# Optimization experiments

Measured on AMD Instinct MI355X. Metric: run time of the kernel, lower is better.

Reference implementation:

```python
import jax, jax.numpy as jnp
import numpy as np

B, T, D = 4, 2048, 512
H, DK = 4, 16
MU = 1.0


def _xavier(key, shape):
    lim = float(np.sqrt(6.0 / (shape[0] + shape[1])))
    return jax.random.uniform(key, shape, jnp.float32, -lim, lim)


def setup_inputs() -> dict:
    key = jax.random.key(0)
    ks = jax.random.split(key, 9)
    x = jax.random.normal(ks[0], (B, T, D), jnp.float32)
    Wq = _xavier(ks[1], (D, H * DK))
    Wk = _xavier(ks[2], (D, H * DK))
    Wv = _xavier(ks[3], (D, H * DK))
    # W_a is zero-initialized in the module; use small random values so the
    # decay path is exercised non-trivially.
    Wa = 0.02 * jax.random.normal(ks[4], (D, H), jnp.float32)
    ba = 0.02 * jax.random.normal(ks[5], (H,), jnp.float32)
    Wg = 0.02 * jax.random.normal(ks[6], (D, H * DK), jnp.float32)
    bg = jnp.zeros((H * DK,), jnp.float32)
    Wo = _xavier(ks[7], (H * DK, D))
    return {"x": x, "Wq": Wq, "Wk": Wk, "Wv": Wv, "Wa": Wa, "ba": ba,
            "Wg": Wg, "bg": bg, "Wo": Wo}


def reference(x, Wq, Wk, Wv, Wa, ba, Wg, bg, Wo):
    b_, t_, _ = x.shape
    q = (x @ Wq).reshape(b_, t_, H, DK)
    k = (x @ Wk).reshape(b_, t_, H, DK)
    v = (x @ Wv).reshape(b_, t_, H, DK)
    # bid b_s = <q_s, k_s>/sqrt(dk); decay a_s = -softplus(x W_a + c_a) <= 0
    bid = jnp.sum(q * k, axis=-1) / np.sqrt(DK)      # (B, T, H)
    a = -jax.nn.softplus(x @ Wa + ba)                # (B, T, H)
    # Closed form of the sequential scan:
    #   scores[t, s] = bid[s] + sum_{r=s+1..t} a[r] = (bid[s] - cumA[s]) + cumA[t]
    # Row-constant cumA[t] cancels in the softmax, so the attention weights are
    # a causal softmax over mu * (bid[s] - cumA[s]).
    cumA = jnp.cumsum(a, axis=1)                     # (B, T, H)
    lg = (bid - cumA).transpose(0, 2, 1)             # (B, H, S_keys)
    mask = jnp.tril(jnp.ones((t_, t_), bool))        # keys s <= query t
    scores = jnp.where(mask[None, None], MU * lg[:, :, None, :], -jnp.inf)
    w = jax.nn.softmax(scores, axis=-1)              # (B, H, T, S)
    y = jnp.einsum('bhts,bshd->bthd', w, v)          # (B, T, H, DK)
    gate = jax.nn.sigmoid(x @ Wg + bg).reshape(b_, t_, H, DK)
    y = (y * gate).reshape(b_, t_, H * DK)
    return y @ Wo
```

## Files before the change

### kernel.cpp

```cpp
#include <hip/hip_runtime.h>
#include <math.h>

#define B_    4
#define T_    2048
#define D_    512
#define H_    4
#define ROWS_ 8192
#define CHSZ_ 128
#define NCHK_ 16

typedef unsigned short ushort_t;
typedef unsigned int   uint_t;
typedef __attribute__((ext_vector_type(8))) __bf16         bfx8;
typedef __attribute__((ext_vector_type(8))) unsigned short u16x8;
typedef __attribute__((ext_vector_type(4))) float          fx4;

__device__ __forceinline__ ushort_t f2bf(float f) {
    union { float f; uint_t u; } v; v.f = f;
    return (ushort_t)((v.u + 0x7FFFu + ((v.u >> 16) & 1u)) >> 16);
}
__device__ __forceinline__ float bf2f(ushort_t u) {
    union { uint_t u; float f; } v; v.u = ((uint_t)u) << 16; return v.f;
}

__global__ __launch_bounds__(256) void prep_pack(const float* __restrict__ x,
                                                 const float* __restrict__ Wa,
                                                 const float* __restrict__ ba,
                                                 const float* __restrict__ Wq,
                                                 const float* __restrict__ Wk,
                                                 const float* __restrict__ Wv,
                                                 const float* __restrict__ Wg,
                                                 const float* __restrict__ Wo,
                                                 ushort_t* __restrict__ xbf,
                                                 float* __restrict__ Aarr,
                                                 ushort_t* __restrict__ WcatT2,
                                                 ushort_t* __restrict__ WoT) {
    const int blk = blockIdx.x;
    if (blk < 2048) {
        const int wave = threadIdx.x >> 6, lane = threadIdx.x & 63;
        const int row = blk * 4 + wave;
        const float* xp = x + (size_t)row * D_ + lane * 8;
        float4 f0 = *(const float4*)xp;
        float4 f1 = *(const float4*)(xp + 4);
        float xv[8] = {f0.x, f0.y, f0.z, f0.w, f1.x, f1.y, f1.z, f1.w};

        u16x8 u;
        #pragma unroll
        for (int j = 0; j < 8; j++) u[j] = f2bf(xv[j]);
        *(u16x8*)(xbf + (size_t)row * D_ + lane * 8) = u;

        float a0 = 0.f, a1 = 0.f, a2 = 0.f, a3 = 0.f;
        #pragma unroll
        for (int j = 0; j < 8; j++) {
            float4 w = *(const float4*)&Wa[(size_t)(lane * 8 + j) * 4];
            a0 = fmaf(xv[j], w.x, a0);
            a1 = fmaf(xv[j], w.y, a1);
            a2 = fmaf(xv[j], w.z, a2);
            a3 = fmaf(xv[j], w.w, a3);
        }
        #pragma unroll
        for (int off = 32; off; off >>= 1) {
            a0 += __shfl_xor(a0, off);
            a1 += __shfl_xor(a1, off);
            a2 += __shfl_xor(a2, off);
            a3 += __shfl_xor(a3, off);
        }
        if (lane == 0) {
            float z[4] = {a0 + ba[0], a1 + ba[1], a2 + ba[2], a3 + ba[3]};
            float r[4];
            #pragma unroll
            for (int h = 0; h < 4; h++)
                r[h] = -(fmaxf(z[h], 0.f) + log1pf(expf(-fabsf(z[h]))));
            *(float4*)&Aarr[(size_t)row * 4] = make_float4(r[0], r[1], r[2], r[3]);
        }
    } else {
        int idx = (blk - 2048) * 256 + threadIdx.x;
        if (idx < 256 * 512) {
            int n = idx >> 9, d = idx & 511;
            int h = n >> 6, r = n & 63, part = r >> 4, j = r & 15;
            int col = h * 16 + j;
            const float* W = (part == 0) ? Wq : (part == 1) ? Wk : (part == 2) ? Wv : Wg;
            WcatT2[idx] = f2bf(W[(size_t)d * 64 + col]);
        } else {
            int r = idx - 256 * 512;
            int n = r >> 6, k = r & 63;
            WoT[r] = f2bf(Wo[(size_t)k * 512 + n]);
        }
    }
}

__global__ __launch_bounds__(256) void gemm_scanA(const ushort_t* __restrict__ xbf,
                                                  const ushort_t* __restrict__ WcatT2,
                                                  const float* __restrict__ Aarr,
                                                  float* __restrict__ stateWS,
                                                  float* __restrict__ chunkSum,
                                                  ushort_t* __restrict__ gBuf) {
    __shared__ ushort_t As[128 * 72];
    __shared__ ushort_t Bs[64 * 72];
    __shared__ float s_a0;
    __shared__ float s_wmax[2];
    __shared__ float s_tot[17];

    const int rc = blockIdx.x & 63;
    const int h  = blockIdx.x >> 6;
    const int m0 = rc * 128;
    const int n0 = h * 64;
    const int b  = rc >> 4, chunk = rc & 15;
    const int bh = b * 4 + h;

    const int tid = threadIdx.x;
    const int wave = tid >> 6, lane = tid & 63;
    const int fr = lane & 15, quad = lane >> 4;
    const int sr = tid >> 3, sc = (tid & 7) * 8;

    fx4 acc[2][4];
    #pragma unroll
    for (int i = 0; i < 2; i++)
        #pragma unroll
        for (int j = 0; j < 4; j++) acc[i][j] = (fx4)0.f;

    u16x8 ra[4], rb[2];
    #pragma unroll
    for (int s = 0; s < 4; s++)
        ra[s] = *(const u16x8*)(xbf + (size_t)(m0 + s * 32 + sr) * D_ + sc);
    #pragma unroll
    for (int s = 0; s < 2; s++)
        rb[s] = *(const u16x8*)(WcatT2 + (size_t)(n0 + s * 32 + sr) * D_ + sc);

    for (int it = 0; it < 8; it++) {
        #pragma unroll
        for (int s = 0; s < 4; s++) *(u16x8*)&As[(s * 32 + sr) * 72 + sc] = ra[s];
        #pragma unroll
        for (int s = 0; s < 2; s++) *(u16x8*)&Bs[(s * 32 + sr) * 72 + sc] = rb[s];
        __syncthreads();
        if (it < 7) {
            const int k0 = (it + 1) * 64;
            #pragma unroll
            for (int s = 0; s < 4; s++)
                ra[s] = *(const u16x8*)(xbf + (size_t)(m0 + s * 32 + sr) * D_ + k0 + sc);
            #pragma unroll
            for (int s = 0; s < 2; s++)
                rb[s] = *(const u16x8*)(WcatT2 + (size_t)(n0 + s * 32 + sr) * D_ + k0 + sc);
        }
        #pragma unroll
        for (int ks = 0; ks < 64; ks += 32) {
            bfx8 af[2], bfr[4];
            #pragma unroll
            for (int mi = 0; mi < 2; mi++)
                af[mi] = *(const bfx8*)&As[(wave * 32 + mi * 16 + fr) * 72 + ks + quad * 8];
            #pragma unroll
            for (int ni = 0; ni < 4; ni++)
                bfr[ni] = *(const bfx8*)&Bs[(ni * 16 + fr) * 72 + ks + quad * 8];
            #pragma unroll
            for (int mi = 0; mi < 2; mi++)
                #pragma unroll
                for (int ni = 0; ni < 4; ni++)
                    acc[mi][ni] = __builtin_amdgcn_mfma_f32_16x16x32_bf16(af[mi], bfr[ni], acc[mi][ni], 0, 0, 0);
        }
        __syncthreads();
    }

    #pragma unroll
    for (int mi = 0; mi < 2; mi++)
        #pragma unroll
        for (int ni = 0; ni < 4; ni++)
            #pragma unroll
            for (int r = 0; r < 4; r++) {
                int rl = wave * 32 + mi * 16 + quad * 4 + r;
                int cl = ni * 16 + fr;
                As[rl * 72 + cl] = f2bf(acc[mi][ni][r]);
            }
    __syncthreads();

    const bool active = (tid < 128);
    float bid = 0.f, a = 0.f;
    float v[16];
    if (active) {
        const ushort_t* ct = &As[tid * 72];
        u16x8 q0 = *(const u16x8*)(ct +  0), q1 = *(const u16x8*)(ct +  8);
        u16x8 k0 = *(const u16x8*)(ct + 16), k1 = *(const u16x8*)(ct + 24);
        u16x8 v0 = *(const u16x8*)(ct + 32), v1 = *(const u16x8*)(ct + 40);
        #pragma unroll
        for (int j = 0; j < 8; j++) {
            bid = fmaf(bf2f(q0[j]), bf2f(k0[j]), bid);
            bid = fmaf(bf2f(q1[j]), bf2f(k1[j]), bid);
            v[j]     = bf2f(v0[j]);
            v[8 + j] = bf2f(v1[j]);
        }
        bid *= 0.25f;
        a = Aarr[(size_t)(m0 + tid) * 4 + h];
    }

    float ca = a;
    #pragma unroll
    for (int off = 1; off < 64; off <<= 1) {
        float up = __shfl_up(ca, off);
        if (lane >= off) ca += up;
    }
    if (tid == 63) s_a0 = ca;
    __syncthreads();
    if (active && wave == 1) ca += s_a0;

    float lg = bid - ca;

    float Mw = active ? lg : -1e30f;
    #pragma unroll
    for (int off = 32; off; off >>= 1) Mw = fmaxf(Mw, __shfl_xor(Mw, off));
    if (active && lane == 0) s_wmax[wave] = Mw;
    __syncthreads();
    const float M0 = s_wmax[0], M1 = s_wmax[1];
    const float Mc = fmaxf(M0, M1);

    float d = active ? __expf(lg - Mw) : 0.f;
    float n[16];
    #pragma unroll
    for (int j = 0; j < 16; j++) n[j] = d * v[j];
    #pragma unroll
    for (int off = 1; off < 64; off <<= 1) {
        float ud = __shfl_up(d, off);
        float un[16];
        #pragma unroll
        for (int j = 0; j < 16; j++) un[j] = __shfl_up(n[j], off);
        if (lane >= off) {
            d += ud;
            #pragma unroll
            for (int j = 0; j < 16; j++) n[j] += un[j];
        }
    }
    if (tid == 63) {
        s_tot[0] = d;
        #pragma unroll
        for (int j = 0; j < 16; j++) s_tot[1 + j] = n[j];
    }
    __syncthreads();
    if (active && wave == 1) {
        float al = __expf(M0 - Mc), be = __expf(M1 - Mc);
        d = s_tot[0] * al + d * be;
        #pragma unroll
        for (int j = 0; j < 16; j++) n[j] = s_tot[1 + j] * al + n[j] * be;
    }
    const float myM = (wave == 0) ? M0 : Mc;

    if (active) {
        const int t = chunk * CHSZ_ + tid;
        const size_t eidx = (size_t)bh * T_ + t;
        stateWS[eidx] = myM;
        stateWS[32768 + eidx] = d;
        #pragma unroll
        for (int j = 0; j < 16; j++) stateWS[(size_t)(2 + j) * 32768 + eidx] = n[j];

        const ushort_t* ct = &As[tid * 72];
        u16x8 g0 = *(const u16x8*)(ct + 48), g1 = *(const u16x8*)(ct + 56);
        *(u16x8*)(gBuf + eidx * 16)     = g0;
        *(u16x8*)(gBuf + eidx * 16 + 8) = g1;

        if (tid == 127) {
            float* cs = chunkSum + (size_t)(bh * NCHK_ + chunk) * 20;
            cs[0] = Mc; cs[1] = d;
            #pragma unroll
            for (int j = 0; j < 16; j++) cs[2 + j] = n[j];
            cs[18] = ca;
        }
    }
}

__global__ __launch_bounds__(256) void scan_gemm(const float* __restrict__ stateWS,
                                                 const float* __restrict__ chunkSum,
                                                 const ushort_t* __restrict__ gBuf,
                                                 const float* __restrict__ bg,
                                                 const ushort_t* __restrict__ WoT,
                                                 float* __restrict__ C) {
    __shared__ ushort_t Ys[64 * 72];
    __shared__ ushort_t Bs[128 * 72];
    __shared__ float s_pref[4][18];

    const int m0 = blockIdx.y * 64;
    const int n0 = blockIdx.x * 128;
    const int b  = m0 >> 11;
    const int tt = m0 & 2047;
    const int chunk = tt >> 7;

    const int tid = threadIdx.x;
    const int wave = tid >> 6, lane = tid & 63;

    const int sr = tid >> 3, sc = (tid & 7) * 8;
    #pragma unroll
    for (int s = 0; s < 4; s++) {
        int rr = s * 32 + sr;
        *(u16x8*)&Bs[rr * 72 + sc] = *(const u16x8*)(WoT + (size_t)(n0 + rr) * 64 + sc);
    }

    const int h = wave, r = lane;
    const int bh = b * 4 + h;
    const size_t eidx = (size_t)bh * T_ + tt + r;
    float m_row = stateWS[eidx];
    float d_row = stateWS[32768 + eidx];
    float n_row[16];
    #pragma unroll
    for (int j = 0; j < 16; j++) n_row[j] = stateWS[(size_t)(2 + j) * 32768 + eidx];
    u16x8 g0 = *(const u16x8*)(gBuf + eidx * 16);
    u16x8 g1 = *(const u16x8*)(gBuf + eidx * 16 + 8);

    if (wave == 0) {
        const int hh = lane >> 4, p = lane & 15;
        const int bhh = b * 4 + hh;
        float mf = -1e30f, dd = 0.f, aT = 0.f;
        float nn[16];
        #pragma unroll
        for (int j = 0; j < 16; j++) nn[j] = 0.f;
        if (p < chunk) {
            const float* cs = chunkSum + (size_t)(bhh * NCHK_ + p) * 20;
            mf = cs[0]; dd = cs[1];
            #pragma unroll
            for (int j = 0; j < 16; j++) nn[j] = cs[2 + j];
            aT = cs[18];
        }
        float off = aT;
        #pragma unroll
        for (int s = 1; s < 16; s <<= 1) {
            float t2 = __shfl_down(off, s, 16);
            if (p + s < chunk) off += t2;
        }
        if (p < chunk) mf += off;
        #pragma unroll
        for (int s = 1; s < 16; s <<= 1) {
            float m2 = __shfl_xor(mf, s, 16);
            float d2 = __shfl_xor(dd, s, 16);
            float mx = fmaxf(mf, m2);
            float al = __expf(mf - mx), be = __expf(m2 - mx);
            #pragma unroll
            for (int j = 0; j < 16; j++) {
                float n2 = __shfl_xor(nn[j], s, 16);
                nn[j] = nn[j] * al + n2 * be;
            }
            dd = dd * al + d2 * be;
            mf = mx;
        }
        if (p == 0) {
            s_pref[hh][0] = mf; s_pref[hh][1] = dd;
            #pragma unroll
            for (int j = 0; j < 16; j++) s_pref[hh][2 + j] = nn[j];
        }
    }
    __syncthreads();

    {
        const float M = s_pref[h][0], D = s_pref[h][1];
        const float mx = fmaxf(M, m_row);
        const float al = __expf(M - mx), be = __expf(m_row - mx);
        const float invd = 1.f / (D * al + d_row * be);
        u16x8 o0, o1;
        #pragma unroll
        for (int j = 0; j < 16; j++) {
            float Nj = s_pref[h][2 + j] * al + n_row[j] * be;
            float gpre = ((j < 8) ? bf2f(g0[j]) : bf2f(g1[j - 8])) + bg[h * 16 + j];
            float gate = 1.f / (1.f + __expf(-gpre));
            ushort_t yb = f2bf(Nj * invd * gate);
            if (j < 8) o0[j] = yb; else o1[j - 8] = yb;
        }
        *(u16x8*)&Ys[r * 72 + h * 16]     = o0;
        *(u16x8*)&Ys[r * 72 + h * 16 + 8] = o1;
    }
    __syncthreads();

    const int wr = wave >> 1, wc = wave & 1;
    const int fr = lane & 15, quad = lane >> 4;
    fx4 acc[2][4];
    #pragma unroll
    for (int i = 0; i < 2; i++)
        #pragma unroll
        for (int j = 0; j < 4; j++) acc[i][j] = (fx4)0.f;

    #pragma unroll
    for (int ks = 0; ks < 64; ks += 32) {
        bfx8 af[2], bfr[4];
        #pragma unroll
        for (int mi = 0; mi < 2; mi++)
            af[mi] = *(const bfx8*)&Ys[(wr * 32 + mi * 16 + fr) * 72 + ks + quad * 8];
        #pragma unroll
        for (int ni = 0; ni < 4; ni++)
            bfr[ni] = *(const bfx8*)&Bs[(wc * 64 + ni * 16 + fr) * 72 + ks + quad * 8];
        #pragma unroll
        for (int mi = 0; mi < 2; mi++)
            #pragma unroll
            for (int ni = 0; ni < 4; ni++)
                acc[mi][ni] = __builtin_amdgcn_mfma_f32_16x16x32_bf16(af[mi], bfr[ni], acc[mi][ni], 0, 0, 0);
    }

    #pragma unroll
    for (int mi = 0; mi < 2; mi++)
        #pragma unroll
        for (int ni = 0; ni < 4; ni++)
            #pragma unroll
            for (int rr = 0; rr < 4; rr++) {
                int orow = m0 + wr * 32 + mi * 16 + quad * 4 + rr;
                int ocol = n0 + wc * 64 + ni * 16 + fr;
                C[(size_t)orow * D_ + ocol] = acc[mi][ni][rr];
            }
}

extern "C" void kernel_launch(void* const* d_in, const int* in_sizes, int n_in,
                              void* d_out, int out_size, void* d_ws, size_t ws_size,
                              hipStream_t stream) {
    const float* x  = (const float*)d_in[0];
    const float* Wq = (const float*)d_in[1];
    const float* Wk = (const float*)d_in[2];
    const float* Wv = (const float*)d_in[3];
    const float* Wa = (const float*)d_in[4];
    const float* ba = (const float*)d_in[5];
    const float* Wg = (const float*)d_in[6];
    const float* bg = (const float*)d_in[7];
    const float* Wo = (const float*)d_in[8];
    float* out = (float*)d_out;

    char* w = (char*)d_ws;
    ushort_t* xbf      = (ushort_t*)w;  w += (size_t)ROWS_ * D_ * 2;
    ushort_t* WcatT2   = (ushort_t*)w;  w += 256 * 512 * 2;
    ushort_t* WoT      = (ushort_t*)w;  w += 512 * 64 * 2;
    float*    Aarr     = (float*)w;     w += (size_t)ROWS_ * 4 * 4;
    float*    stateWS  = (float*)w;     w += (size_t)18 * 32768 * 4;
    float*    chunkSum = (float*)w;     w += 256 * 20 * 4;
    ushort_t* gBuf     = (ushort_t*)w;  w += (size_t)32768 * 16 * 2;

    prep_pack<<<2688, 256, 0, stream>>>(x, Wa, ba, Wq, Wk, Wv, Wg, Wo,
                                        xbf, Aarr, WcatT2, WoT);
    gemm_scanA<<<256, 256, 0, stream>>>(xbf, WcatT2, Aarr, stateWS, chunkSum, gBuf);
    scan_gemm<<<dim3(4, 128), 256, 0, stream>>>(stateWS, chunkSum, gBuf, bg, WoT, out);
}
```

Baseline: 111.5 us.

## Fuse bf16 packing and decay projection into the GEMM kernels, drop prep kernel

Removes the separate prep_pack launch. The QKVG GEMM now loads fp32 x and the weights directly, converts them to bf16 while staging into shared memory, and accumulates the x·Wa decay projection on the fly with a shuffle reduction. The output GEMM converts Wo to bf16 from strided fp32 reads. This saves a kernel launch and the round trip of the xbf and A buffers through global memory. In exchange, each block reads fp32 x at twice the bytes, and the weight loads are uncoalesced scalar strided accesses repeated across blocks.

```diff
diff --git a/kernel.cpp b/kernel.cpp
--- a/kernel.cpp
+++ b/kernel.cpp
@@ -23,80 +23,19 @@
     union { uint_t u; float f; } v; v.u = ((uint_t)u) << 16; return v.f;
 }
 
-__global__ __launch_bounds__(256) void prep_pack(const float* __restrict__ x,
-                                                 const float* __restrict__ Wa,
-                                                 const float* __restrict__ ba,
-                                                 const float* __restrict__ Wq,
-                                                 const float* __restrict__ Wk,
-                                                 const float* __restrict__ Wv,
-                                                 const float* __restrict__ Wg,
-                                                 const float* __restrict__ Wo,
-                                                 ushort_t* __restrict__ xbf,
-                                                 float* __restrict__ Aarr,
-                                                 ushort_t* __restrict__ WcatT2,
-                                                 ushort_t* __restrict__ WoT) {
-    const int blk = blockIdx.x;
-    if (blk < 2048) {
-        const int wave = threadIdx.x >> 6, lane = threadIdx.x & 63;
-        const int row = blk * 4 + wave;
-        const float* xp = x + (size_t)row * D_ + lane * 8;
-        float4 f0 = *(const float4*)xp;
-        float4 f1 = *(const float4*)(xp + 4);
-        float xv[8] = {f0.x, f0.y, f0.z, f0.w, f1.x, f1.y, f1.z, f1.w};
-
-        u16x8 u;
-        #pragma unroll
-        for (int j = 0; j < 8; j++) u[j] = f2bf(xv[j]);
-        *(u16x8*)(xbf + (size_t)row * D_ + lane * 8) = u;
-
-        float a0 = 0.f, a1 = 0.f, a2 = 0.f, a3 = 0.f;
-        #pragma unroll
-        for (int j = 0; j < 8; j++) {
-            float4 w = *(const float4*)&Wa[(size_t)(lane * 8 + j) * 4];
-            a0 = fmaf(xv[j], w.x, a0);
-            a1 = fmaf(xv[j], w.y, a1);
-            a2 = fmaf(xv[j], w.z, a2);
-            a3 = fmaf(xv[j], w.w, a3);
-        }
-        #pragma unroll
-        for (int off = 32; off; off >>= 1) {
-            a0 += __shfl_xor(a0, off);
-            a1 += __shfl_xor(a1, off);
-            a2 += __shfl_xor(a2, off);
-            a3 += __shfl_xor(a3, off);
-        }
-        if (lane == 0) {
-            float z[4] = {a0 + ba[0], a1 + ba[1], a2 + ba[2], a3 + ba[3]};
-            float r[4];
-            #pragma unroll
-            for (int h = 0; h < 4; h++)
-                r[h] = -(fmaxf(z[h], 0.f) + log1pf(expf(-fabsf(z[h]))));
-            *(float4*)&Aarr[(size_t)row * 4] = make_float4(r[0], r[1], r[2], r[3]);
-        }
-    } else {
-        int idx = (blk - 2048) * 256 + threadIdx.x;
-        if (idx < 256 * 512) {
-            int n = idx >> 9, d = idx & 511;
-            int h = n >> 6, r = n & 63, part = r >> 4, j = r & 15;
-            int col = h * 16 + j;
-            const float* W = (part == 0) ? Wq : (part == 1) ? Wk : (part == 2) ? Wv : Wg;
-            WcatT2[idx] = f2bf(W[(size_t)d * 64 + col]);
-        } else {
-            int r = idx - 256 * 512;
-            int n = r >> 6, k = r & 63;
-            WoT[r] = f2bf(Wo[(size_t)k * 512 + n]);
-        }
-    }
-}
-
-__global__ __launch_bounds__(256) void gemm_scanA(const ushort_t* __restrict__ xbf,
-                                                  const ushort_t* __restrict__ WcatT2,
-                                                  const float* __restrict__ Aarr,
+__global__ __launch_bounds__(256) void gemm_scanA(const float* __restrict__ x,
+                                                  const float* __restrict__ Wa,
+                                                  const float* __restrict__ ba,
+                                                  const float* __restrict__ Wq,
+                                                  const float* __restrict__ Wk,
+                                                  const float* __restrict__ Wv,
+                                                  const float* __restrict__ Wg,
                                                   float* __restrict__ stateWS,
                                                   float* __restrict__ chunkSum,
                                                   ushort_t* __restrict__ gBuf) {
     __shared__ ushort_t As[128 * 72];
     __shared__ ushort_t Bs[64 * 72];
+    __shared__ float s_a[128];
     __shared__ float s_a0;
     __shared__ float s_wmax[2];
     __shared__ float s_tot[17];
@@ -104,7 +43,6 @@
     const int rc = blockIdx.x & 63;
     const int h  = blockIdx.x >> 6;
     const int m0 = rc * 128;
-    const int n0 = h * 64;
     const int b  = rc >> 4, chunk = rc & 15;
     const int bh = b * 4 + h;
 
@@ -113,34 +51,69 @@
     const int fr = lane & 15, quad = lane >> 4;
     const int sr = tid >> 3, sc = (tid & 7) * 8;
 
+    const int colw = h * 16 + (sr & 15);
+    const float* W1 = (sr < 16) ? Wq : Wk;
+    const float* W2 = (sr < 16) ? Wv : Wg;
+
     fx4 acc[2][4];
     #pragma unroll
     for (int i = 0; i < 2; i++)
         #pragma unroll
         for (int j = 0; j < 4; j++) acc[i][j] = (fx4)0.f;
 
-    u16x8 ra[4], rb[2];
-    #pragma unroll
-    for (int s = 0; s < 4; s++)
-        ra[s] = *(const u16x8*)(xbf + (size_t)(m0 + s * 32 + sr) * D_ + sc);
-    #pragma unroll
-    for (int s = 0; s < 2; s++)
-        rb[s] = *(const u16x8*)(WcatT2 + (size_t)(n0 + s * 32 + sr) * D_ + sc);
+    float pa[4] = {0.f, 0.f, 0.f, 0.f};
+
+    float4 raF[4][2];
+    float  rbF[2][8];
+    float  rwa[8];
+    #pragma unroll
+    for (int s = 0; s < 4; s++) {
+        const float* xp = x + (size_t)(m0 + s * 32 + sr) * D_ + sc;
+        raF[s][0] = *(const float4*)xp;
+        raF[s][1] = *(const float4*)(xp + 4);
+    }
+    #pragma unroll
+    for (int j = 0; j < 8; j++) {
+        rbF[0][j] = W1[(size_t)(sc + j) * 64 + colw];
+        rbF[1][j] = W2[(size_t)(sc + j) * 64 + colw];
+        rwa[j]    = Wa[(size_t)(sc + j) * 4 + h];
+    }
 
     for (int it = 0; it < 8; it++) {
         #pragma unroll
-        for (int s = 0; s < 4; s++) *(u16x8*)&As[(s * 32 + sr) * 72 + sc] = ra[s];
-        #pragma unroll
-        for (int s = 0; s < 2; s++) *(u16x8*)&Bs[(s * 32 + sr) * 72 + sc] = rb[s];
+        for (int s = 0; s < 4; s++) {
+            float xv[8] = {raF[s][0].x, raF[s][0].y, raF[s][0].z, raF[s][0].w,
+                           raF[s][1].x, raF[s][1].y, raF[s][1].z, raF[s][1].w};
+            u16x8 u;
+            #pragma unroll
+            for (int j = 0; j < 8; j++) {
+                u[j] = f2bf(xv[j]);
+                pa[s] = fmaf(xv[j], rwa[j], pa[s]);
+            }
+            *(u16x8*)&As[(s * 32 + sr) * 72 + sc] = u;
+        }
+        #pragma unroll
+        for (int s = 0; s < 2; s++) {
+            u16x8 u;
+            #pragma unroll
+            for (int j = 0; j < 8; j++) u[j] = f2bf(rbF[s][j]);
+            *(u16x8*)&Bs[(s * 32 + sr) * 72 + sc] = u;
+        }
         __syncthreads();
         if (it < 7) {
             const int k0 = (it + 1) * 64;
             #pragma unroll
-            for (int s = 0; s < 4; s++)
-                ra[s] = *(const u16x8*)(xbf + (size_t)(m0 + s * 32 + sr) * D_ + k0 + sc);
-            #pragma unroll
-            for (int s = 0; s < 2; s++)
-                rb[s] = *(const u16x8*)(WcatT2 + (size_t)(n0 + s * 32 + sr) * D_ + k0 + sc);
+            for (int s = 0; s < 4; s++) {
+                const float* xp = x + (size_t)(m0 + s * 32 + sr) * D_ + k0 + sc;
+                raF[s][0] = *(const float4*)xp;
+                raF[s][1] = *(const float4*)(xp + 4);
+            }
+            #pragma unroll
+            for (int j = 0; j < 8; j++) {
+                rbF[0][j] = W1[(size_t)(k0 + sc + j) * 64 + colw];
+                rbF[1][j] = W2[(size_t)(k0 + sc + j) * 64 + colw];
+                rwa[j]    = Wa[(size_t)(k0 + sc + j) * 4 + h];
+            }
         }
         #pragma unroll
         for (int ks = 0; ks < 64; ks += 32) {
@@ -170,6 +143,20 @@
                 int cl = ni * 16 + fr;
                 As[rl * 72 + cl] = f2bf(acc[mi][ni][r]);
             }
+
+    #pragma unroll
+    for (int s = 0; s < 4; s++) {
+        #pragma unroll
+        for (int m = 1; m < 8; m <<= 1) pa[s] += __shfl_xor(pa[s], m, 8);
+    }
+    if ((tid & 7) == 0) {
+        const float bah = ba[h];
+        #pragma unroll
+        for (int s = 0; s < 4; s++) {
+            float z = pa[s] + bah;
+            s_a[s * 32 + sr] = -(fmaxf(z, 0.f) + log1pf(expf(-fabsf(z))));
+        }
+    }
     __syncthreads();
 
     const bool active = (tid < 128);
@@ -188,7 +175,7 @@
             v[8 + j] = bf2f(v1[j]);
         }
         bid *= 0.25f;
-        a = Aarr[(size_t)(m0 + tid) * 4 + h];
+        a = s_a[tid];
     }
 
     float ca = a;
@@ -268,7 +255,7 @@
                                                  const float* __restrict__ chunkSum,
                                                  const ushort_t* __restrict__ gBuf,
                                                  const float* __restrict__ bg,
-                                                 const ushort_t* __restrict__ WoT,
+                                                 const float* __restrict__ Wo,
                                                  float* __restrict__ C) {
     __shared__ ushort_t Ys[64 * 72];
     __shared__ ushort_t Bs[128 * 72];
@@ -287,7 +274,11 @@
     #pragma unroll
     for (int s = 0; s < 4; s++) {
         int rr = s * 32 + sr;
-        *(u16x8*)&Bs[rr * 72 + sc] = *(const u16x8*)(WoT + (size_t)(n0 + rr) * 64 + sc);
+        u16x8 u;
+        #pragma unroll
+        for (int j = 0; j < 8; j++)
+            u[j] = f2bf(Wo[(size_t)(sc + j) * D_ + n0 + rr]);
+        *(u16x8*)&Bs[rr * 72 + sc] = u;
     }
 
     const int h = wave, r = lane;
@@ -414,16 +405,11 @@
     float* out = (float*)d_out;
 
     char* w = (char*)d_ws;
-    ushort_t* xbf      = (ushort_t*)w;  w += (size_t)ROWS_ * D_ * 2;
-    ushort_t* WcatT2   = (ushort_t*)w;  w += 256 * 512 * 2;
-    ushort_t* WoT      = (ushort_t*)w;  w += 512 * 64 * 2;
-    float*    Aarr     = (float*)w;     w += (size_t)ROWS_ * 4 * 4;
     float*    stateWS  = (float*)w;     w += (size_t)18 * 32768 * 4;
     float*    chunkSum = (float*)w;     w += 256 * 20 * 4;
     ushort_t* gBuf     = (ushort_t*)w;  w += (size_t)32768 * 16 * 2;
 
-    prep_pack<<<2688, 256, 0, stream>>>(x, Wa, ba, Wq, Wk, Wv, Wg, Wo,
-                                        xbf, Aarr, WcatT2, WoT);
-    gemm_scanA<<<256, 256, 0, stream>>>(xbf, WcatT2, Aarr, stateWS, chunkSum, gBuf);
-    scan_gemm<<<dim3(4, 128), 256, 0, stream>>>(stateWS, chunkSum, gBuf, bg, WoT, out);
+    gemm_scanA<<<256, 256, 0, stream>>>(x, Wa, ba, Wq, Wk, Wv, Wg,
+                                        stateWS, chunkSum, gBuf);
+    scan_gemm<<<dim3(4, 128), 256, 0, stream>>>(stateWS, chunkSum, gBuf, bg, Wo, out);
 }
```

New measurement: 114.4 us. +2.6%, slower.
